# Optimization experiments

Hardware: AMD Instinct MI355X
Metric: run time of the kernel (lower is better)

## Reference

```python
import jax, jax.numpy as jnp
import numpy as np

IN_F, OUT_F = 768, 2304
E, R = 8, 16            # num adapters, lora rank
ALPHA = 32
SCALING = ALPHA / R
GATE_DIM = 64


def setup_inputs() -> dict:
    key = jax.random.key(0)
    ks = jax.random.split(key, 8)
    B, S = 8, 2048
    x = jax.random.normal(ks[0], (B, S, IN_F), dtype=jnp.float32)
    z = jax.random.normal(ks[1], (B, GATE_DIM), dtype=jnp.float32)
    # frozen linear (nn.Linear weight layout [out, in])
    W = jax.random.normal(ks[2], (OUT_F, IN_F), dtype=jnp.float32) * 0.02
    b = jax.random.normal(ks[3], (OUT_F,), dtype=jnp.float32) * 0.02
    # stacked LoRA adapters: A [E, r, in], B [E, out, r]
    A = jax.random.normal(ks[4], (E, R, IN_F), dtype=jnp.float32) * (1.0 / np.sqrt(IN_F))
    Bm = jax.random.normal(ks[5], (E, OUT_F, R), dtype=jnp.float32) * 0.02
    # spectral gate: linear + softmax over experts
    Wg = jax.random.normal(ks[6], (E, GATE_DIM), dtype=jnp.float32) * 0.1
    bg = jax.random.normal(ks[7], (E,), dtype=jnp.float32) * 0.1
    return {"x": x, "z": z, "W": W, "b": b, "A": A, "Bm": Bm, "Wg": Wg, "bg": bg}


def reference(x, z, W, b, A, Bm, Wg, bg):
    # frozen linear: [B,S,out]
    frozen_out = jnp.einsum('bsi,oi->bso', x, W) + b
    # gate weights over adapters: [B,E]
    gate_w = jax.nn.softmax(jnp.einsum('bg,eg->be', z, Wg) + bg, axis=-1)
    # fused adapters: down-proj to rank r per expert (dropout p=0 -> identity)
    h = jnp.einsum('bsi,eri->bser', x, A)               # [B,S,E,r] small (r=16)
    # up-proj + gate-weighted sum over experts, fused into one contraction
    adapt = jnp.einsum('bser,eor,be->bso', h, Bm, gate_w) * SCALING
    return frozen_out + adapt
```

## Files before the change

### kernel.cpp

```cpp
#include <hip/hip_runtime.h>
#include <hip/hip_bf16.h>
#include <stdint.h>

typedef unsigned short u16;
typedef __attribute__((ext_vector_type(8))) short short8;
typedef __attribute__((ext_vector_type(4))) float floatx4;

#define M_TOT 16384
#define N_OUT 2304
#define KX    768
#define KL    128
#define SCALING 2.0f

#define XBLKS   6144
#define WBLKS   864
#define ABLKS   48
#define BMRBLKS 144
#define PREP_BLOCKS (XBLKS + WBLKS + ABLKS + BMRBLKS + 1)

__device__ __forceinline__ u16 f2b(float f) {
  union { __hip_bfloat16 h; u16 u; } c; c.h = __float2bfloat16(f); return c.u;
}
__device__ __forceinline__ float ldf(const void* p, long i, bool f32) {
  if (f32) return ((const float*)p)[i];
  union { u16 u; __hip_bfloat16 h; } c; c.u = ((const u16*)p)[i];
  return __bfloat162float(c.h);
}

__device__ __forceinline__ void gload_lds16(const void* g, void* l) {
  __builtin_amdgcn_global_load_lds(
      (const __attribute__((address_space(1))) void*)g,
      (__attribute__((address_space(3))) void*)l, 16, 0, 0);
}

__device__ __forceinline__ void cvt8(const void* src, u16* dst, long i, bool f32) {
  u16 v[8];
  if (f32) {
    const float4* s = (const float4*)src;
    float4 a = s[i * 2], b = s[i * 2 + 1];
    v[0] = f2b(a.x); v[1] = f2b(a.y); v[2] = f2b(a.z); v[3] = f2b(a.w);
    v[4] = f2b(b.x); v[5] = f2b(b.y); v[6] = f2b(b.z); v[7] = f2b(b.w);
  } else {
    *(uint4*)v = ((const uint4*)src)[i];
  }
  ((uint4*)dst)[i] = *(uint4*)v;
}

__global__ __launch_bounds__(256) void prep_kernel(
    const void* __restrict__ x,  const void* __restrict__ W,
    const void* __restrict__ A,  const void* __restrict__ Bm,
    const void* __restrict__ z,  const void* __restrict__ Wg,
    const void* __restrict__ bg,
    u16* __restrict__ xbf, u16* __restrict__ Wbf, u16* __restrict__ Abf,
    u16* __restrict__ bmr, float* __restrict__ gsc, int* __restrict__ flagp) {
  __shared__ int s_flag;
  const int tid = threadIdx.x;
  if (tid < 64) {
    u16 v = ((const u16*)x)[tid * 2];
    int e = (v >> 7) & 0xFF;
    int huge = (e >= 160) ? 1 : 0;
    for (int off = 1; off < 64; off <<= 1) huge += __shfl_xor(huge, off, 64);
    if (tid == 0) s_flag = (huge >= 4) ? 1 : 0;
  }
  __syncthreads();
  const bool f32 = (s_flag != 0);

  int b = blockIdx.x;
  if (b < XBLKS) {
    cvt8(x, xbf, (long)b * 256 + tid, f32);
  } else if (b < XBLKS + WBLKS) {
    cvt8(W, Wbf, (long)(b - XBLKS) * 256 + tid, f32);
  } else if (b < XBLKS + WBLKS + ABLKS) {
    cvt8(A, Abf, (long)(b - XBLKS - WBLKS) * 256 + tid, f32);
  } else if (b < XBLKS + WBLKS + ABLKS + BMRBLKS) {
    long i0 = ((long)(b - XBLKS - WBLKS - ABLKS) * 256 + tid) * 8;
    u16 v[8];
#pragma unroll
    for (int j = 0; j < 8; ++j) {
      long idx = i0 + j;
      long o = idx >> 7, er = idx & 127;
      long e = er >> 4, r = er & 15;
      v[j] = f2b(ldf(Bm, (e * 2304 + o) * 16 + r, f32));
    }
    *(uint4*)&bmr[i0] = *(uint4*)v;
  } else {
    if (tid == 0) *flagp = s_flag;
    if (tid < 64) {
      const int bb = tid >> 3, e = tid & 7;
      float acc = ldf(bg, e, f32);
      for (int i = 0; i < 64; ++i)
        acc += ldf(z, bb * 64 + i, f32) * ldf(Wg, e * 64 + i, f32);
      float mx = acc;
      for (int off = 1; off < 8; off <<= 1) mx = fmaxf(mx, __shfl_xor(mx, off, 64));
      float ex = __expf(acc - mx);
      float sm = ex;
      for (int off = 1; off < 8; off <<= 1) sm += __shfl_xor(sm, off, 64);
      gsc[tid] = (ex / sm) * SCALING;
    }
  }
}

__global__ __launch_bounds__(256) void gemm_h(
    const u16* __restrict__ xbf, const u16* __restrict__ Abf,
    const float* __restrict__ gsc, u16* __restrict__ hg) {
  __shared__ __align__(128) u16 As[64][64];
  __shared__ __align__(128) u16 Bs[128][64];
  const int tid = threadIdx.x, wave = tid >> 6, lane = tid & 63;
  const int wm = wave >> 1, wn = wave & 1;
  const int quad = lane >> 4, l16 = lane & 15;
  const int srow = lane >> 3, scol = (lane & 7) * 8;
  const int m0 = blockIdx.x * 64;

  floatx4 acc[2][4];
#pragma unroll
  for (int i = 0; i < 2; ++i)
#pragma unroll
    for (int j = 0; j < 4; ++j) acc[i][j] = floatx4{0.f, 0.f, 0.f, 0.f};

  for (int kb = 0; kb < 12; ++kb) {
    const int kc = kb * 64;
#pragma unroll
    for (int j = 0; j < 2; ++j) {
      int r = wave * 16 + j * 8 + srow;
      gload_lds16(xbf + (size_t)(m0 + r) * KX + kc + scol,
                  (char*)(&As[0][0]) + (wave * 16 + j * 8) * 128);
    }
#pragma unroll
    for (int j = 0; j < 4; ++j) {
      int r = wave * 32 + j * 8 + srow;
      gload_lds16(Abf + (size_t)r * KX + kc + scol,
                  (char*)(&Bs[0][0]) + (wave * 32 + j * 8) * 128);
    }
    __syncthreads();
#pragma unroll
    for (int ks = 0; ks < 2; ++ks) {
      short8 af[2], bf[4];
#pragma unroll
      for (int mi = 0; mi < 2; ++mi)
        af[mi] = *(const short8*)&As[wm * 32 + mi * 16 + l16][ks * 32 + quad * 8];
#pragma unroll
      for (int ni = 0; ni < 4; ++ni)
        bf[ni] = *(const short8*)&Bs[wn * 64 + ni * 16 + l16][ks * 32 + quad * 8];
#pragma unroll
      for (int mi = 0; mi < 2; ++mi)
#pragma unroll
        for (int ni = 0; ni < 4; ++ni)
          acc[mi][ni] = __builtin_amdgcn_mfma_f32_16x16x32_bf16(af[mi], bf[ni], acc[mi][ni], 0, 0, 0);
    }
    __syncthreads();
  }
  const int bb = m0 >> 11;
  float gv[4];
#pragma unroll
  for (int ni = 0; ni < 4; ++ni) gv[ni] = gsc[bb * 8 + wn * 4 + ni];
#pragma unroll
  for (int mi = 0; mi < 2; ++mi) {
    int rbase = m0 + wm * 32 + mi * 16 + quad * 4;
#pragma unroll
    for (int ni = 0; ni < 4; ++ni) {
      int c = wn * 64 + ni * 16 + l16;
#pragma unroll
      for (int t = 0; t < 4; ++t)
        hg[(size_t)(rbase + t) * KL + c] = f2b(acc[mi][ni][t] * gv[ni]);
    }
  }
}

__global__ __launch_bounds__(256) void gemm_main(
    const u16* __restrict__ xbf, const u16* __restrict__ hg,
    const u16* __restrict__ Wbf, const u16* __restrict__ bmr,
    const void* __restrict__ bias, void* __restrict__ outv,
    const int* __restrict__ flagp) {
  __shared__ __align__(128) u16 As[128][64];
  __shared__ __align__(128) u16 Bs[128][64];
  __shared__ u16 occ_pad[4096];
  const int tid = threadIdx.x, wave = tid >> 6, lane = tid & 63;
  const int wm = wave >> 1, wn = wave & 1;
  const int quad = lane >> 4, l16 = lane & 15;
  const int srow = lane >> 3, scol = (lane & 7) * 8;

  const int linear = blockIdx.x;
  const int xcd = linear & 7;
  const int g = linear >> 3;
  const int st = g / 24;
  const int w  = g % 24;
  const int m_idx = xcd * 16 + (st / 6) * 8 + (w & 7);
  const int n_idx = (st % 6) * 3 + (w >> 3);
  const int m0 = m_idx * 128;
  const int n0 = n_idx * 128;
  if (tid == 0) ((volatile u16*)occ_pad)[0] = (u16)linear;

  floatx4 acc[4][4];
#pragma unroll
  for (int i = 0; i < 4; ++i)
#pragma unroll
    for (int j = 0; j < 4; ++j) acc[i][j] = floatx4{0.f, 0.f, 0.f, 0.f};

  for (int kb = 0; kb < 14; ++kb) {
    const u16* ap; const u16* bp; int lda, ldb, kc;
    if (kb < 12) { ap = xbf; lda = KX; bp = Wbf; ldb = KX; kc = kb * 64; }
    else         { ap = hg;  lda = KL; bp = bmr; ldb = KL; kc = (kb - 12) * 64; }
#pragma unroll
    for (int j = 0; j < 4; ++j) {
      int r = wave * 32 + j * 8 + srow;
      gload_lds16(ap + (size_t)(m0 + r) * lda + kc + scol,
                  (char*)(&As[0][0]) + (wave * 32 + j * 8) * 128);
      gload_lds16(bp + (size_t)(n0 + r) * ldb + kc + scol,
                  (char*)(&Bs[0][0]) + (wave * 32 + j * 8) * 128);
    }
    __syncthreads();
#pragma unroll
    for (int ks = 0; ks < 2; ++ks) {
      short8 af[4], bf[4];
#pragma unroll
      for (int mi = 0; mi < 4; ++mi)
        af[mi] = *(const short8*)&As[wm * 64 + mi * 16 + l16][ks * 32 + quad * 8];
#pragma unroll
      for (int ni = 0; ni < 4; ++ni)
        bf[ni] = *(const short8*)&Bs[wn * 64 + ni * 16 + l16][ks * 32 + quad * 8];
#pragma unroll
      for (int mi = 0; mi < 4; ++mi)
#pragma unroll
        for (int ni = 0; ni < 4; ++ni)
          acc[mi][ni] = __builtin_amdgcn_mfma_f32_16x16x32_bf16(af[mi], bf[ni], acc[mi][ni], 0, 0, 0);
    }
    __syncthreads();
  }

  const bool f32 = (*flagp != 0);
  float bv[4];
#pragma unroll
  for (int ni = 0; ni < 4; ++ni)
    bv[ni] = ldf(bias, n0 + wn * 64 + ni * 16 + l16, f32);
#pragma unroll
  for (int mi = 0; mi < 4; ++mi) {
    int rbase = m0 + wm * 64 + mi * 16 + quad * 4;
#pragma unroll
    for (int ni = 0; ni < 4; ++ni) {
      int c = n0 + wn * 64 + ni * 16 + l16;
#pragma unroll
      for (int t = 0; t < 4; ++t) {
        float v = acc[mi][ni][t] + bv[ni];
        size_t idx = (size_t)(rbase + t) * N_OUT + c;
        if (f32) __builtin_nontemporal_store(v, (float*)outv + idx);
        else     __builtin_nontemporal_store(f2b(v), (u16*)outv + idx);
      }
    }
  }
}

extern "C" void kernel_launch(void* const* d_in, const int* in_sizes, int n_in,
                              void* d_out, int out_size, void* d_ws, size_t ws_size,
                              hipStream_t stream) {
  const void* x  = d_in[0];
  const void* z  = d_in[1];
  const void* W  = d_in[2];
  const void* bb = d_in[3];
  const void* A  = d_in[4];
  const void* Bm = d_in[5];
  const void* Wg = d_in[6];
  const void* bg = d_in[7];

  char* ws = (char*)d_ws;
  int*   flag = (int*)ws;
  float* gsc  = (float*)(ws + 256);
  u16*   xbf  = (u16*)(ws + 1024);
  u16*   Wbf  = (u16*)(ws + 1024 + 25165824ull);
  u16*   Abf  = (u16*)(ws + 1024 + 25165824ull + 3538944ull);
  u16*   bmr  = (u16*)(ws + 1024 + 25165824ull + 3538944ull + 196608ull);
  u16*   hg   = (u16*)(ws + 1024 + 25165824ull + 3538944ull + 196608ull + 589824ull);

  prep_kernel<<<PREP_BLOCKS, 256, 0, stream>>>(
      x, W, A, Bm, z, Wg, bg, xbf, Wbf, Abf, bmr, gsc, flag);

  gemm_h<<<M_TOT / 64, 256, 0, stream>>>(xbf, Abf, gsc, hg);

  gemm_main<<<(N_OUT / 128) * (M_TOT / 128), 256, 0, stream>>>(
      xbf, hg, Wbf, bmr, bb, d_out, flag);
}
```

Baseline: 128.1 us.

## Fuse x bf16 conversion into gemm_h and vectorize output stores via transposed MFMA

```diff
diff --git a/kernel.cpp b/kernel.cpp
--- a/kernel.cpp
+++ b/kernel.cpp
@@ -5,6 +5,7 @@
 typedef unsigned short u16;
 typedef __attribute__((ext_vector_type(8))) short short8;
 typedef __attribute__((ext_vector_type(4))) float floatx4;
+typedef unsigned int __attribute__((ext_vector_type(2))) uint2v;
 
 #define M_TOT 16384
 #define N_OUT 2304
@@ -12,11 +13,10 @@
 #define KL    128
 #define SCALING 2.0f
 
-#define XBLKS   6144
 #define WBLKS   864
 #define ABLKS   48
 #define BMRBLKS 144
-#define PREP_BLOCKS (XBLKS + WBLKS + ABLKS + BMRBLKS + 1)
+#define PREP_BLOCKS (WBLKS + ABLKS + BMRBLKS + 1)
 
 __device__ __forceinline__ u16 f2b(float f) {
   union { __hip_bfloat16 h; u16 u; } c; c.h = __float2bfloat16(f); return c.u;
@@ -51,7 +51,7 @@
     const void* __restrict__ A,  const void* __restrict__ Bm,
     const void* __restrict__ z,  const void* __restrict__ Wg,
     const void* __restrict__ bg,
-    u16* __restrict__ xbf, u16* __restrict__ Wbf, u16* __restrict__ Abf,
+    u16* __restrict__ Wbf, u16* __restrict__ Abf,
     u16* __restrict__ bmr, float* __restrict__ gsc, int* __restrict__ flagp) {
   __shared__ int s_flag;
   const int tid = threadIdx.x;
@@ -66,14 +66,12 @@
   const bool f32 = (s_flag != 0);
 
   int b = blockIdx.x;
-  if (b < XBLKS) {
-    cvt8(x, xbf, (long)b * 256 + tid, f32);
-  } else if (b < XBLKS + WBLKS) {
-    cvt8(W, Wbf, (long)(b - XBLKS) * 256 + tid, f32);
-  } else if (b < XBLKS + WBLKS + ABLKS) {
-    cvt8(A, Abf, (long)(b - XBLKS - WBLKS) * 256 + tid, f32);
-  } else if (b < XBLKS + WBLKS + ABLKS + BMRBLKS) {
-    long i0 = ((long)(b - XBLKS - WBLKS - ABLKS) * 256 + tid) * 8;
+  if (b < WBLKS) {
+    cvt8(W, Wbf, (long)b * 256 + tid, f32);
+  } else if (b < WBLKS + ABLKS) {
+    cvt8(A, Abf, (long)(b - WBLKS) * 256 + tid, f32);
+  } else if (b < WBLKS + ABLKS + BMRBLKS) {
+    long i0 = ((long)(b - WBLKS - ABLKS) * 256 + tid) * 8;
     u16 v[8];
 #pragma unroll
     for (int j = 0; j < 8; ++j) {
@@ -101,8 +99,9 @@
 }
 
 __global__ __launch_bounds__(256) void gemm_h(
-    const u16* __restrict__ xbf, const u16* __restrict__ Abf,
-    const float* __restrict__ gsc, u16* __restrict__ hg) {
+    const void* __restrict__ x, const u16* __restrict__ Abf,
+    const float* __restrict__ gsc, u16* __restrict__ xbf,
+    u16* __restrict__ hg, const int* __restrict__ flagp) {
   __shared__ __align__(128) u16 As[64][64];
   __shared__ __align__(128) u16 Bs[128][64];
   const int tid = threadIdx.x, wave = tid >> 6, lane = tid & 63;
@@ -110,6 +109,10 @@
   const int quad = lane >> 4, l16 = lane & 15;
   const int srow = lane >> 3, scol = (lane & 7) * 8;
   const int m0 = blockIdx.x * 64;
+  const bool f32 = (*flagp != 0);
+
+  const int xr = tid >> 2, cg16 = (tid & 3) * 16;
+  char* Asb = (char*)&As[0][0];
 
   floatx4 acc[2][4];
 #pragma unroll
@@ -119,11 +122,27 @@
 
   for (int kb = 0; kb < 12; ++kb) {
     const int kc = kb * 64;
-#pragma unroll
-    for (int j = 0; j < 2; ++j) {
-      int r = wave * 16 + j * 8 + srow;
-      gload_lds16(xbf + (size_t)(m0 + r) * KX + kc + scol,
-                  (char*)(&As[0][0]) + (wave * 16 + j * 8) * 128);
+    {
+      const long off = (long)(m0 + xr) * KX + kc + cg16;
+      uint4 lo, hi;
+      if (f32) {
+        const float4* xs = (const float4*)((const float*)x + off);
+        float4 f0 = xs[0], f1 = xs[1], f2c = xs[2], f3 = xs[3];
+        u16 v[16];
+        v[0] = f2b(f0.x); v[1] = f2b(f0.y); v[2]  = f2b(f0.z); v[3]  = f2b(f0.w);
+        v[4] = f2b(f1.x); v[5] = f2b(f1.y); v[6]  = f2b(f1.z); v[7]  = f2b(f1.w);
+        v[8] = f2b(f2c.x); v[9] = f2b(f2c.y); v[10] = f2b(f2c.z); v[11] = f2b(f2c.w);
+        v[12] = f2b(f3.x); v[13] = f2b(f3.y); v[14] = f2b(f3.z); v[15] = f2b(f3.w);
+        lo = *(uint4*)&v[0]; hi = *(uint4*)&v[8];
+      } else {
+        lo = *(const uint4*)&((const u16*)x)[off];
+        hi = *(const uint4*)&((const u16*)x)[off + 8];
+      }
+      *(uint4*)&xbf[off] = lo;
+      *(uint4*)&xbf[off + 8] = hi;
+      const int cb = cg16 * 2, sw = (xr & 7) << 4;
+      *(uint4*)(Asb + xr * 128 + ((cb +  0) ^ sw)) = lo;
+      *(uint4*)(Asb + xr * 128 + ((cb + 16) ^ sw)) = hi;
     }
 #pragma unroll
     for (int j = 0; j < 4; ++j) {
@@ -136,8 +155,10 @@
     for (int ks = 0; ks < 2; ++ks) {
       short8 af[2], bf[4];
 #pragma unroll
-      for (int mi = 0; mi < 2; ++mi)
-        af[mi] = *(const short8*)&As[wm * 32 + mi * 16 + l16][ks * 32 + quad * 8];
+      for (int mi = 0; mi < 2; ++mi) {
+        int ar = wm * 32 + mi * 16 + l16;
+        af[mi] = *(const short8*)(Asb + ar * 128 + ((ks * 64 + quad * 16) ^ ((ar & 7) << 4)));
+      }
 #pragma unroll
       for (int ni = 0; ni < 4; ++ni)
         bf[ni] = *(const short8*)&Bs[wn * 64 + ni * 16 + l16][ks * 32 + quad * 8];
@@ -222,28 +243,37 @@
       for (int mi = 0; mi < 4; ++mi)
 #pragma unroll
         for (int ni = 0; ni < 4; ++ni)
-          acc[mi][ni] = __builtin_amdgcn_mfma_f32_16x16x32_bf16(af[mi], bf[ni], acc[mi][ni], 0, 0, 0);
+          acc[mi][ni] = __builtin_amdgcn_mfma_f32_16x16x32_bf16(bf[ni], af[mi], acc[mi][ni], 0, 0, 0);
     }
     __syncthreads();
   }
 
   const bool f32 = (*flagp != 0);
-  float bv[4];
-#pragma unroll
-  for (int ni = 0; ni < 4; ++ni)
-    bv[ni] = ldf(bias, n0 + wn * 64 + ni * 16 + l16, f32);
 #pragma unroll
   for (int mi = 0; mi < 4; ++mi) {
-    int rbase = m0 + wm * 64 + mi * 16 + quad * 4;
+    const size_t row = (size_t)(m0 + wm * 64 + mi * 16 + l16);
 #pragma unroll
     for (int ni = 0; ni < 4; ++ni) {
-      int c = n0 + wn * 64 + ni * 16 + l16;
-#pragma unroll
-      for (int t = 0; t < 4; ++t) {
-        float v = acc[mi][ni][t] + bv[ni];
-        size_t idx = (size_t)(rbase + t) * N_OUT + c;
-        if (f32) __builtin_nontemporal_store(v, (float*)outv + idx);
-        else     __builtin_nontemporal_store(f2b(v), (u16*)outv + idx);
+      const int c0 = n0 + wn * 64 + ni * 16 + quad * 4;
+      float b0, b1, b2, b3;
+      if (f32) {
+        const float4 bv = *(const float4*)((const float*)bias + c0);
+        b0 = bv.x; b1 = bv.y; b2 = bv.z; b3 = bv.w;
+      } else {
+        b0 = ldf(bias, c0, false);     b1 = ldf(bias, c0 + 1, false);
+        b2 = ldf(bias, c0 + 2, false); b3 = ldf(bias, c0 + 3, false);
+      }
+      const float v0 = acc[mi][ni][0] + b0, v1 = acc[mi][ni][1] + b1;
+      const float v2 = acc[mi][ni][2] + b2, v3 = acc[mi][ni][3] + b3;
+      if (f32) {
+        floatx4 v = {v0, v1, v2, v3};
+        __builtin_nontemporal_store(
+            v, (floatx4*)((float*)outv + row * N_OUT + c0));
+      } else {
+        union { u16 h[4]; uint2v u; } pk;
+        pk.h[0] = f2b(v0); pk.h[1] = f2b(v1); pk.h[2] = f2b(v2); pk.h[3] = f2b(v3);
+        __builtin_nontemporal_store(
+            pk.u, (uint2v*)((u16*)outv + row * N_OUT + c0));
       }
     }
   }
@@ -271,9 +301,9 @@
   u16*   hg   = (u16*)(ws + 1024 + 25165824ull + 3538944ull + 196608ull + 589824ull);
 
   prep_kernel<<<PREP_BLOCKS, 256, 0, stream>>>(
-      x, W, A, Bm, z, Wg, bg, xbf, Wbf, Abf, bmr, gsc, flag);
-
-  gemm_h<<<M_TOT / 64, 256, 0, stream>>>(xbf, Abf, gsc, hg);
+      x, W, A, Bm, z, Wg, bg, Wbf, Abf, bmr, gsc, flag);
+
+  gemm_h<<<M_TOT / 64, 256, 0, stream>>>(x, Abf, gsc, xbf, hg, flag);
 
   gemm_main<<<(N_OUT / 128) * (M_TOT / 128), 256, 0, stream>>>(
       xbf, hg, Wbf, bmr, bb, d_out, flag);
```

New measurement: 129.9 us. Within noise of the previous version (+1.4%).
